# Kernel tuning notes

Hardware: AMD Instinct MI355X
Metric: run time of the kernel (lower is better)

Reference implementation:

```python
import jax, jax.numpy as jnp
import numpy as np

B = 64       # number of graphs (regular batching)
NPER = 2048  # nodes per graph
K = 16       # kNN neighbors (includes self, as torch_cluster.knn does)
D_IN = 64
D_OUT = 64


def setup_inputs() -> dict:
    key = jax.random.key(0)
    k1, k2 = jax.random.split(key, 2)
    x = jax.random.normal(k1, (B * NPER, D_IN), jnp.float32)
    batch = jnp.repeat(jnp.arange(B, dtype=jnp.int32), NPER)
    # MLP: Linear(2*in_channels, out_channels, bias=True) + ReLU
    weight = jax.random.normal(k2, (D_OUT, 2 * D_IN), jnp.float32) * (1.0 / np.sqrt(2 * D_IN))
    bias = jnp.zeros((D_OUT,), jnp.float32)
    return {"x": x, "batch": batch, "weight": weight, "bias": bias}


def reference(x, batch, weight, bias):
    # batch is a regular assignment (NPER nodes per graph) -> block the kNN per graph
    d = x.shape[1]
    xb = x.reshape(B, NPER, d)                                   # [B, n, d]
    # squared euclidean distances within each graph
    sq = jnp.sum(xb * xb, axis=-1)                               # [B, n]
    dist = sq[:, :, None] + sq[:, None, :] - 2.0 * jnp.einsum('bnd,bmd->bnm', xb, xb)
    # k nearest (smallest distance); self-distance 0 -> self included, matching PyG knn
    _, idx = jax.lax.top_k(-dist, K)                             # [B, n, K]
    xj = jax.vmap(lambda feats, ids: feats[ids])(xb, idx)        # [B, n, K, d]
    xi = xb[:, :, None, :]                                        # [B, n, 1, d]
    msg = jnp.concatenate([jnp.broadcast_to(xi, xj.shape), xj - xi], axis=-1)  # [B,n,K,2d]
    h = jax.nn.relu(jnp.einsum('bnkf,of->bnko', msg, weight) + bias)
    out = jnp.max(h, axis=2)                                      # max aggregation over neighbors
    return out.reshape(B * NPER, -1)
```

## Files before the change

kernel.cpp:

```cpp
#include <hip/hip_runtime.h>
#include <cfloat>

#define BB 64
#define NPERB 2048
#define KNN 16
#define NTOT (BB*NPERB)
#define NCAND 24

typedef __bf16 bf16x8 __attribute__((ext_vector_type(8)));
typedef float  f32x4  __attribute__((ext_vector_type(4)));

__device__ __forceinline__ unsigned int med3u(unsigned int a, unsigned int b, unsigned int c) {
    unsigned int d;
    asm("v_med3_u32 %0, %1, %2, %3" : "=v"(d) : "v"(a), "v"(b), "v"(c));
    return d;
}

__device__ __forceinline__ unsigned short bf16rn(float f) {
    unsigned int u = __float_as_uint(f);
    u += 0x7fffu + ((u >> 16) & 1u);
    return (unsigned short)(u >> 16);
}
__device__ __forceinline__ unsigned int pk2(float a, float b) {
    return ((unsigned int)bf16rn(b) << 16) | (unsigned int)bf16rn(a);
}

__global__ __launch_bounds__(256) void k_transform(const float4* __restrict__ x4,
    const float* __restrict__ w, const float* __restrict__ bias,
    float* __restrict__ Aout, float* __restrict__ Bvv, float* __restrict__ sqnp,
    uint4* __restrict__ xbu4)
{
    __shared__ __align__(16) float wm[64*64];
    __shared__ __align__(16) float w2m[64*64];
    const int t = threadIdx.x;
    const int r = blockIdx.x * 256 + t;

#pragma unroll
    for (int i = 0; i < 16; ++i) {
        int e = t + i*256;
        int o = e >> 6, f = e & 63;
        float w1 = w[o*128 + f];
        float w2 = w[o*128 + 64 + f];
        wm[e]  = w1 - w2;
        w2m[e] = w2;
    }

    float xr[64];
#pragma unroll
    for (int j = 0; j < 16; ++j) {
        float4 v = x4[(size_t)r * 16 + j];
        xr[4*j+0] = v.x; xr[4*j+1] = v.y; xr[4*j+2] = v.z; xr[4*j+3] = v.w;
    }

    {
        float rr[8];
#pragma unroll
        for (int j = 0; j < 8; ++j) rr[j] = __fmul_rn(xr[j], xr[j]);
#pragma unroll
        for (int i = 1; i < 8; ++i)
#pragma unroll
            for (int j = 0; j < 8; ++j)
                rr[j] = __fadd_rn(rr[j], __fmul_rn(xr[8*i + j], xr[8*i + j]));
        float t01 = __fadd_rn(rr[0], rr[1]);
        float t23 = __fadd_rn(rr[2], rr[3]);
        float t45 = __fadd_rn(rr[4], rr[5]);
        float t67 = __fadd_rn(rr[6], rr[7]);
        sqnp[r] = __fadd_rn(__fadd_rn(t01, t23), __fadd_rn(t45, t67));
    }

#pragma unroll
    for (int i = 0; i < 8; ++i) {
        uint4 u;
        u.x = pk2(xr[8*i+0], xr[8*i+1]);
        u.y = pk2(xr[8*i+2], xr[8*i+3]);
        u.z = pk2(xr[8*i+4], xr[8*i+5]);
        u.w = pk2(xr[8*i+6], xr[8*i+7]);
        xbu4[(size_t)r * 8 + i] = u;
    }

    __syncthreads();

    for (int o = 0; o < 64; o += 4) {
        float a4[4], b4[4];
#pragma unroll
        for (int oo = 0; oo < 4; ++oo) {
            const float* wmr  = &wm [(o + oo)*64];
            const float* w2mr = &w2m[(o + oo)*64];
            float a1 = 0.f, a2 = 0.f;
#pragma unroll
            for (int fi = 0; fi < 16; ++fi) {
                f32x4 wa = *(const f32x4*)&wmr [fi*4];
                f32x4 wb = *(const f32x4*)&w2mr[fi*4];
#pragma unroll
                for (int k = 0; k < 4; ++k) {
                    float xv = xr[fi*4 + k];
                    a1 = __builtin_fmaf(xv, wa[k], a1);
                    a2 = __builtin_fmaf(xv, wb[k], a2);
                }
            }
            a4[oo] = __fadd_rn(a1, bias[o + oo]);
            b4[oo] = a2;
        }
        *(float4*)&Aout[(size_t)r * 64 + o] = make_float4(a4[0], a4[1], a4[2], a4[3]);
        *(float4*)&Bvv [(size_t)r * 64 + o] = make_float4(b4[0], b4[1], b4[2], b4[3]);
    }
}

__global__ __launch_bounds__(256, 5) void k_topk(const float4* __restrict__ x4,
    const uint4* __restrict__ xb, const float* __restrict__ sq, int* __restrict__ nbr)
{
    __shared__ __align__(16) char smem[28160];
    unsigned short* bsh0 = (unsigned short*)smem;
    unsigned short* bsh1 = (unsigned short*)(smem + 9216);
    unsigned short* rsh  = (unsigned short*)(smem + 18432);
    float* sqc           = (float*)(smem + 27648);
    unsigned int* cand   = (unsigned int*)smem;
    unsigned short* cand24 = (unsigned short*)(smem + 17408);

    int t = threadIdx.x;
    int lane = t & 63;
    int w = t >> 6;
    int ln = lane & 15, qd = lane >> 4;
    int batch = blockIdx.x >> 5;
    int strip = blockIdx.x & 31;
    int rbase = batch * NPERB;
    int r0g = rbase + strip * 64;

    unsigned int ks[16];
#pragma unroll
    for (int j = 0; j < 16; ++j) ks[j] = 0xFFFFFFFFu;

    auto issue_load = [&](int ct_, uint4& p0, uint4& p1, float& sp) {
        const uint4* src = xb + ((size_t)rbase + ct_*64) * 8;
        p0 = src[t]; p1 = src[t + 256];
        sp = (t < 64) ? sq[rbase + ct_*64 + t] : 0.f;
    };
    auto stage_write = [&](int ct_, uint4 p0, uint4 p1, float sp) {
        unsigned short* bnext = ((ct_ + 1) & 1) ? bsh1 : bsh0;
        *(uint4*)&bnext[(t >> 3)*72 + (t & 7)*8] = p0;
        int l1 = t + 256;
        *(uint4*)&bnext[(l1 >> 3)*72 + (l1 & 7)*8] = p1;
        if (t < 64) sqc[((ct_ + 1) & 1)*64 + t] = sp;
    };

    {
        const uint4* src = xb + (size_t)r0g * 8;
#pragma unroll
        for (int i = 0; i < 2; ++i) {
            int l = t + i*256;
            uint4 v = src[l];
            *(uint4*)&rsh[(l >> 3)*72 + (l & 7)*8] = v;
        }
    }
    uint4 pA0, pA1, pB0, pB1; float sA, sB;
    issue_load(0, pA0, pA1, sA);
    __syncthreads();
    bf16x8 rf0 = *(const bf16x8*)&rsh[(w*16 + ln)*72 + qd*8];
    bf16x8 rf1 = *(const bf16x8*)&rsh[(w*16 + ln)*72 + 32 + qd*8];
    float sqr16 = sq[r0g + w*16 + ln] + 16.f;

    stage_write(-1, pA0, pA1, sA);
    issue_load(1, pA0, pA1, sA);
    __syncthreads();

    auto compute_tile = [&](int ct_, const unsigned short* bcur, const float* sqcur) {
#pragma unroll
        for (int ct2 = 0; ct2 < 4; ++ct2) {
            int pt = ct2*16 + ln;
            bf16x8 a0 = *(const bf16x8*)&bcur[pt*72 + qd*8];
            bf16x8 a1 = *(const bf16x8*)&bcur[pt*72 + 32 + qd*8];
            f32x4 acc = {0.f, 0.f, 0.f, 0.f};
            acc = __builtin_amdgcn_mfma_f32_16x16x32_bf16(a0, rf0, acc, 0, 0, 0);
            acc = __builtin_amdgcn_mfma_f32_16x16x32_bf16(a1, rf1, acc, 0, 0, 0);
            f32x4 sc4 = *(const f32x4*)&sqcur[ct2*16 + qd*4];
            int idxb = ct_*64 + ct2*16 + qd*4;
#pragma unroll
            for (int j = 0; j < 4; ++j) {
                float s = fmaf(-2.f, acc[j], sc4[j] + sqr16);
                unsigned int u = (__float_as_uint(s) & 0xFFFFF800u) | (unsigned int)(idxb + j);
#pragma unroll
                for (int jj = 15; jj >= 1; --jj) ks[jj] = med3u(u, ks[jj-1], ks[jj]);
                ks[0] = min(ks[0], u);
            }
        }
    };

    for (int ct = 0; ct < 32; ct += 2) {
        if (ct + 2 <= 31) issue_load(ct + 2, pB0, pB1, sB);
        compute_tile(ct, bsh0, sqc);
        stage_write(ct, pA0, pA1, sA);
        __syncthreads();
        if (ct + 3 <= 31) issue_load(ct + 3, pA0, pA1, sA);
        compute_tile(ct + 1, bsh1, sqc + 64);
        if (ct + 1 < 31) stage_write(ct + 1, pB0, pB1, sB);
        __syncthreads();
    }

    {
        int r = w*16 + ln;
#pragma unroll
        for (int j = 0; j < 16; ++j) cand[r*68 + qd*16 + j] = ks[j];
    }
    __syncthreads();

    if (t < 64) {
        unsigned int m24[NCAND];
#pragma unroll
        for (int j = 0; j < NCAND; ++j) m24[j] = 0xFFFFFFFFu;
        for (int i = 0; i < 64; ++i) {
            unsigned int u = cand[t*68 + i];
#pragma unroll
            for (int jj = NCAND-1; jj >= 1; --jj) m24[jj] = med3u(u, m24[jj-1], m24[jj]);
            m24[0] = min(m24[0], u);
        }
#pragma unroll
        for (int j = 0; j < NCAND; ++j) cand24[t*NCAND + j] = (unsigned short)(m24[j] & 0x7FFu);
    }
    __syncthreads();

    {
        int r = t & 63, grp = t >> 6;
        float sqr = sq[r0g + r];
        float4 xrA[8];
#pragma unroll
        for (int i = 0; i < 8; ++i) xrA[i] = x4[(size_t)(r0g + r)*16 + i];
        float* kdf = (float*)cand;
#pragma unroll
        for (int m6 = 0; m6 < 6; ++m6) {
            int m = grp*6 + m6;
            int c = (int)cand24[r*NCAND + m];
            const float4* xb4 = &x4[(size_t)(rbase + c)*16];
            float dot = 0.f;
#pragma unroll
            for (int i = 0; i < 8; ++i) {
                float4 a = xrA[i]; float4 b = xb4[i];
                dot = fmaf(a.x, b.x, dot); dot = fmaf(a.y, b.y, dot);
                dot = fmaf(a.z, b.z, dot); dot = fmaf(a.w, b.w, dot);
            }
#pragma unroll
            for (int i = 8; i < 16; ++i) {
                float4 a = x4[(size_t)(r0g + r)*16 + i]; float4 b = xb4[i];
                dot = fmaf(a.x, b.x, dot); dot = fmaf(a.y, b.y, dot);
                dot = fmaf(a.z, b.z, dot); dot = fmaf(a.w, b.w, dot);
            }
            float kd = __fsub_rn(__fadd_rn(sqr, sq[rbase + c]), __fmul_rn(2.0f, dot));
            kdf[r*68 + m] = kd;
            cand[r*68 + 32 + m] = (unsigned int)c;
        }
    }
    __syncthreads();

    if (t < 64) {
        float* kdf = (float*)cand;
        float dk[KNN]; int di[KNN];
#pragma unroll
        for (int j = 0; j < KNN; ++j) { dk[j] = FLT_MAX; di[j] = 0x7fffffff; }
        for (int m = 0; m < NCAND; ++m) {
            float kd = kdf[t*68 + m];
            int c = (int)cand[t*68 + 32 + m];
            bool better = (kd < dk[KNN-1]) || (kd == dk[KNN-1] && c < di[KNN-1]);
            if (better) {
#pragma unroll
                for (int j = KNN-1; j >= 1; --j) {
                    bool sh = (dk[j-1] > kd) || (dk[j-1] == kd && di[j-1] > c);
                    bool pl = (!sh) && ((dk[j] > kd) || (dk[j] == kd && di[j] > c));
                    float nk = sh ? dk[j-1] : (pl ? kd : dk[j]);
                    int ni = sh ? di[j-1] : (pl ? c : di[j]);
                    dk[j] = nk; di[j] = ni;
                }
                if ((dk[0] > kd) || (dk[0] == kd && di[0] > c)) { dk[0] = kd; di[0] = c; }
            }
        }
#pragma unroll
        for (int k = 0; k < KNN; ++k) nbr[(size_t)(r0g + t)*16 + k] = di[k];
    }
}

__global__ __launch_bounds__(256) void k_combine(const float* __restrict__ Bvv,
    const int* __restrict__ nbr, float* __restrict__ out)
{
    int t = threadIdx.x;
    int row = blockIdx.x*4 + (t >> 6);
    int o = t & 63;
    int rb = (row >> 11) << 11;
    float m = -FLT_MAX;
#pragma unroll
    for (int k = 0; k < 16; ++k) {
        int c = nbr[(size_t)row*16 + k];
        m = fmaxf(m, Bvv[(size_t)(rb + c)*64 + o]);
    }
    out[(size_t)row*64 + o] = fmaxf(out[(size_t)row*64 + o] + m, 0.f);
}

extern "C" void kernel_launch(void* const* d_in, const int* in_sizes, int n_in,
                              void* d_out, int out_size, void* d_ws, size_t ws_size,
                              hipStream_t stream) {
    const float* x    = (const float*)d_in[0];
    const float* w    = (const float*)d_in[2];
    const float* bias = (const float*)d_in[3];
    float* out = (float*)d_out;

    float* Bvv  = (float*)d_ws;
    float* sqnp = Bvv + (size_t)NTOT * 64;
    int*   nbr  = (int*)(sqnp + NTOT);
    unsigned int* xbu = (unsigned int*)(nbr + (size_t)NTOT * 16);

    k_transform<<<NTOT/256, 256, 0, stream>>>((const float4*)x, w, bias, out, Bvv, sqnp, (uint4*)xbu);
    k_topk<<<2048, 256, 0, stream>>>((const float4*)x, (const uint4*)xbu, sqnp, nbr);
    k_combine<<<NTOT/4, 256, 0, stream>>>(Bvv, nbr, out);
}
```

Baseline: 530.9 us.

## Restructure transform GEMM so each lane owns an output column with weights in registers

The per-node linear transform now keeps one output channel's weight column in registers per lane (from a padded, transposed shared buffer) and loops over 64 rows per wavefront, reading x rows with uniform broadcast loads. Output stores become fully coalesced across lanes instead of strided float4 writes per thread. The aim is to remove repeated shared-memory weight reads and uncoalesced stores. The cost is 128 weight registers per thread and x being re-read from global/cache instead of from registers.

```diff
diff --git a/kernel.cpp b/kernel.cpp
--- a/kernel.cpp
+++ b/kernel.cpp
@@ -30,8 +30,8 @@
     float* __restrict__ Aout, float* __restrict__ Bvv, float* __restrict__ sqnp,
     uint4* __restrict__ xbu4)
 {
-    __shared__ __align__(16) float wm[64*64];
-    __shared__ __align__(16) float w2m[64*64];
+    __shared__ __align__(16) float wt1[64*65];
+    __shared__ __align__(16) float wt2[64*65];
     const int t = threadIdx.x;
     const int r = blockIdx.x * 256 + t;
 
@@ -39,10 +39,8 @@
     for (int i = 0; i < 16; ++i) {
         int e = t + i*256;
         int o = e >> 6, f = e & 63;
-        float w1 = w[o*128 + f];
-        float w2 = w[o*128 + 64 + f];
-        wm[e]  = w1 - w2;
-        w2m[e] = w2;
+        wt1[f*65 + o] = w[o*128 + f];
+        wt2[f*65 + o] = w[o*128 + 64 + f];
     }
 
     float xr[64];
@@ -80,29 +78,33 @@
 
     __syncthreads();
 
-    for (int o = 0; o < 64; o += 4) {
-        float a4[4], b4[4];
-#pragma unroll
-        for (int oo = 0; oo < 4; ++oo) {
-            const float* wmr  = &wm [(o + oo)*64];
-            const float* w2mr = &w2m[(o + oo)*64];
-            float a1 = 0.f, a2 = 0.f;
-#pragma unroll
-            for (int fi = 0; fi < 16; ++fi) {
-                f32x4 wa = *(const f32x4*)&wmr [fi*4];
-                f32x4 wb = *(const f32x4*)&w2mr[fi*4];
-#pragma unroll
-                for (int k = 0; k < 4; ++k) {
-                    float xv = xr[fi*4 + k];
-                    a1 = __builtin_fmaf(xv, wa[k], a1);
-                    a2 = __builtin_fmaf(xv, wb[k], a2);
-                }
-            }
-            a4[oo] = __fadd_rn(a1, bias[o + oo]);
-            b4[oo] = a2;
-        }
-        *(float4*)&Aout[(size_t)r * 64 + o] = make_float4(a4[0], a4[1], a4[2], a4[3]);
-        *(float4*)&Bvv [(size_t)r * 64 + o] = make_float4(b4[0], b4[1], b4[2], b4[3]);
+    const int lane = t & 63;
+    const int wv = t >> 6;
+    float wmr[64], w2r[64];
+#pragma unroll
+    for (int f = 0; f < 64; ++f) {
+        float w1v = wt1[f*65 + lane];
+        float w2v = wt2[f*65 + lane];
+        wmr[f] = __fsub_rn(w1v, w2v);
+        w2r[f] = w2v;
+    }
+    const float biasv = bias[lane];
+
+    const int row0 = blockIdx.x * 256 + wv * 64;
+    for (int rr = 0; rr < 64; ++rr) {
+        const int row = row0 + rr;
+        const float4* xrow = x4 + (size_t)row * 16;
+        float a1 = 0.f, a2 = 0.f;
+#pragma unroll
+        for (int j = 0; j < 16; ++j) {
+            float4 xv = xrow[j];
+            a1 = __builtin_fmaf(xv.x, wmr[4*j+0], a1); a2 = __builtin_fmaf(xv.x, w2r[4*j+0], a2);
+            a1 = __builtin_fmaf(xv.y, wmr[4*j+1], a1); a2 = __builtin_fmaf(xv.y, w2r[4*j+1], a2);
+            a1 = __builtin_fmaf(xv.z, wmr[4*j+2], a1); a2 = __builtin_fmaf(xv.z, w2r[4*j+2], a2);
+            a1 = __builtin_fmaf(xv.w, wmr[4*j+3], a1); a2 = __builtin_fmaf(xv.w, w2r[4*j+3], a2);
+        }
+        Aout[(size_t)row*64 + lane] = __fadd_rn(a1, biasv);
+        Bvv [(size_t)row*64 + lane] = a2;
     }
 }
 
```

Measured after the change: 599.1 us. 12.9% more time.
